# Kernel optimization log

Measured on AMD Instinct MI355X. Metric: run time of the kernel, lower is better.

## Reference

```python
import jax, jax.numpy as jnp
import numpy as np

B, L, DIM, S, K = 2, 2048, 1024, 16, 3
INNER = DIM  # expand = 1 (module only runs with expand=1, see notes)


def setup_inputs() -> dict:
    key = jax.random.key(0)
    ks = jax.random.split(key, 10)
    f = lambda k, shape, s=0.02: jax.random.normal(k, shape, jnp.float32) * s
    return {
        "x": jax.random.normal(ks[0], (B, L, DIM), jnp.float32),
        "gamma": jnp.ones((DIM,), jnp.float32),
        "beta": jnp.zeros((DIM,), jnp.float32),
        "W_in": f(ks[1], (2 * INNER, DIM)),
        "conv_w": f(ks[2], (INNER, 1, K), 0.2),   # depthwise conv, OIL layout
        "W_x": f(ks[3], (2 * S, INNER)),
        "W_dt": f(ks[4], (INNER, DIM)),
        "b_dt": f(ks[5], (INNER,), 0.1),
        "A_log": jax.random.normal(ks[6], (INNER, S), jnp.float32),
        "D_param": jnp.ones((INNER,), jnp.float32),
        "W_out": f(ks[7], (DIM, INNER)),
    }


def reference(x, gamma, beta, W_in, conv_w, W_x, W_dt, b_dt, A_log, D_param, W_out):
    residual = x
    # LayerNorm
    mu = jnp.mean(x, axis=-1, keepdims=True)
    var = jnp.var(x, axis=-1, keepdims=True)
    h = (x - mu) / jnp.sqrt(var + 1e-5) * gamma + beta
    # in_proj + chunk
    xz = jnp.einsum('bld,ed->ble', h, W_in)
    inner = W_in.shape[0] // 2
    xx, z = xz[..., :inner], xz[..., inner:]
    # depthwise conv1d, padding (K-1)//2, no bias
    k = conv_w.shape[-1]
    pad = (k - 1) // 2
    xc = jax.lax.conv_general_dilated(
        xx.transpose(0, 2, 1), conv_w, window_strides=(1,),
        padding=[(pad, pad)], dimension_numbers=('NCL', 'OIL', 'NCL'),
        feature_group_count=inner).transpose(0, 2, 1)
    xc = jax.nn.silu(xc)
    # projections for dt, B, C
    dt = jnp.einsum('bld,ed->ble', xc, W_dt) + b_dt
    BC = jnp.einsum('bld,ed->ble', xc, W_x)
    s = A_log.shape[-1]
    Bm, Cm = BC[..., :s], BC[..., s:]
    # selective scan
    A = -jnp.exp(A_log)                               # (d, s)
    dt = jax.nn.softplus(dt)                          # (b, l, d)
    dA = jnp.exp(jnp.einsum('bld,ds->blds', dt, A))   # (b, l, d, s)
    dB = jnp.einsum('bld,bls->blds', dt, Bm)          # (b, l, d, s)

    def step(state, inputs):
        dA_t, dB_t, C_t = inputs                      # (b,d,s), (b,d,s), (b,s)
        state = state * dA_t + dB_t
        y_t = jnp.einsum('bds,bs->bd', state, C_t)
        return state, y_t

    init = jnp.zeros((x.shape[0], inner, s), xc.dtype)
    _, ys = jax.lax.scan(
        step, init,
        (dA.transpose(1, 0, 2, 3), dB.transpose(1, 0, 2, 3), Cm.transpose(1, 0, 2)))
    y = ys.transpose(1, 0, 2)                         # (b, l, d)
    # skip, gate, out projection, residual
    y = y + D_param * xc
    y = y * jax.nn.silu(z)
    out = jnp.einsum('bld,ed->ble', y, W_out)
    return out + residual
```

## Files before the change

kernel.cpp:

```cpp
#include <hip/hip_runtime.h>
#include <math.h>

#define BB 2
#define LL 2048
#define DIMV 1024
#define SSV 16
#define INNERV 1024
#define E2V 2048
#define MMV (BB*LL)
#define NCHUNK 64
#define CLEN 32

typedef __attribute__((ext_vector_type(8))) short short8;
typedef __attribute__((ext_vector_type(4))) float f32x4;

static __device__ __forceinline__ float4 ld4(const float* p){
  return *reinterpret_cast<const float4*>(p);
}
static __device__ __forceinline__ ushort f2bf(float x){
  unsigned u = __float_as_uint(x);
  unsigned r = (u + 0x7fffu + ((u >> 16) & 1u)) >> 16;
  return (ushort)r;
}
static __device__ __forceinline__ float bf2f(ushort h){
  return __uint_as_float(((unsigned)h) << 16);
}
static __device__ __forceinline__ void gld16(const void* g, void* l){
  __builtin_amdgcn_global_load_lds(
      (const __attribute__((address_space(1))) void*)g,
      (__attribute__((address_space(3))) void*)l, 16, 0, 0);
}

static __device__ __forceinline__ int xcd_swz(){
  int bid = blockIdx.y * gridDim.x + blockIdx.x;
  int nwg = gridDim.x * gridDim.y;
  int q = nwg >> 3, r = nwg & 7;
  int xcd = bid & 7, idx = bid >> 3;
  return (xcd < r ? xcd*(q+1) : r*(q+1) + (xcd - r)*q) + idx;
}

__global__ __launch_bounds__(256) void ln_init(
        const float* __restrict__ x, const float* __restrict__ gamma,
        const float* __restrict__ beta, ushort* __restrict__ hh,
        const float* __restrict__ W_in, const float* __restrict__ W_dt,
        const float* __restrict__ W_out, const float* __restrict__ wx,
        ushort* __restrict__ Wih, ushort* __restrict__ Wch,
        ushort* __restrict__ Woh){
  __shared__ float red[8];
  if (blockIdx.x < 4224){
    int idx = blockIdx.x*256 + threadIdx.x;
    if (idx < 1032*1024){
      const float* src; ushort* dst; int i;
      if (idx < 512*1024){ src = W_in;  dst = Wih; i = idx; }
      else if (idx < 768*1024){ src = W_dt;  dst = Wch; i = idx - 512*1024; }
      else if (idx < 1024*1024){ src = W_out; dst = Woh; i = idx - 768*1024; }
      else { src = wx; dst = Wch + (size_t)1024*1024; i = idx - 1024*1024; }
      float4 v = ld4(src + (size_t)i*4);
      ushort4 H;
      H.x=f2bf(v.x); H.y=f2bf(v.y); H.z=f2bf(v.z); H.w=f2bf(v.w);
      *reinterpret_cast<ushort4*>(dst + (size_t)i*4) = H;
    } else {
      int i = idx - 1032*1024;
      *reinterpret_cast<ushort4*>(Wch + (size_t)1056*1024 + (size_t)i*4) =
          make_ushort4(0,0,0,0);
    }
    return;
  }
  int row = blockIdx.x - 4224;
  int tid = threadIdx.x;
  const float* xr = x + (size_t)row*DIMV;
  float4 v = ld4(xr + tid*4);
  float s  = v.x+v.y+v.z+v.w;
  float s2 = v.x*v.x+v.y*v.y+v.z*v.z+v.w*v.w;
  for (int o=32;o;o>>=1){ s += __shfl_down(s,o); s2 += __shfl_down(s2,o); }
  int wid = tid>>6, lane = tid&63;
  if (lane==0){ red[wid]=s; red[4+wid]=s2; }
  __syncthreads();
  s  = red[0]+red[1]+red[2]+red[3];
  s2 = red[4]+red[5]+red[6]+red[7];
  float mu  = s*(1.f/DIMV);
  float var = s2*(1.f/DIMV) - mu*mu;
  float rstd = rsqrtf(var + 1e-5f);
  float4 g = ld4(gamma + tid*4), be = ld4(beta + tid*4);
  ushort4 H;
  H.x = f2bf((v.x-mu)*rstd*g.x + be.x);
  H.y = f2bf((v.y-mu)*rstd*g.y + be.y);
  H.z = f2bf((v.z-mu)*rstd*g.z + be.z);
  H.w = f2bf((v.w-mu)*rstd*g.w + be.w);
  *reinterpret_cast<ushort4*>(hh + (size_t)row*DIMV + tid*4) = H;
}

#define GBK 64
#define NKT 16

template<int EPI>
static __device__ __forceinline__ void gemm_body(ushort* lds,
    const ushort* __restrict__ A, const ushort* __restrict__ Bw,
    void* __restrict__ Co_, int N, const float* __restrict__ aux,
    float* __restrict__ aux2, int bm, int bn){
  const int t  = threadIdx.x;
  const int rr  = t >> 3;
  const int k16 = (t & 7) ^ (rr & 7);
  const ushort* gA = A  + (size_t)(bm + rr)*1024 + k16*8;
  const ushort* gB = Bw + (size_t)(bn + rr)*1024 + k16*8;
  const int wofs = (t >> 6) * 1024;

  const int l  = t & 63, wv = t >> 6;
  const int wm = wv & 1, wn = wv >> 1;
  const int fr = l & 15, kb = l >> 4;

  f32x4 acc[2][2];
  #pragma unroll
  for (int m=0;m<2;m++){
    #pragma unroll
    for (int n=0;n<2;n++) acc[m][n] = (f32x4){0.f,0.f,0.f,0.f};
  }

  char* Lb0 = (char*)lds;
  char* Lb1 = (char*)lds + 16384;

  #define STAGE_T(base, kt_) { \
    const int ko = (kt_)*GBK; \
    gld16(gA + ko,           (base) +     0 + wofs); \
    gld16(gA + ko + 32*1024, (base) +  4096 + wofs); \
    gld16(gB + ko,           (base) +  8192 + wofs); \
    gld16(gB + ko + 32*1024, (base) + 12288 + wofs); }

  #define COMPUTE_T(base) { \
    short8 a[2][2], b[2][2]; \
    _Pragma("unroll") \
    for (int m=0;m<2;m++){ \
      int row = wm*32 + m*16 + fr; \
      _Pragma("unroll") \
      for (int ks=0;ks<2;ks++) \
        a[m][ks] = *(const short8*)((base) + row*128 + (((ks*4+kb)^(fr&7))*16)); \
    } \
    _Pragma("unroll") \
    for (int n=0;n<2;n++){ \
      int row = wn*32 + n*16 + fr; \
      _Pragma("unroll") \
      for (int ks=0;ks<2;ks++) \
        b[n][ks] = *(const short8*)((base) + 8192 + row*128 + (((ks*4+kb)^(fr&7))*16)); \
    } \
    _Pragma("unroll") \
    for (int ks=0;ks<2;ks++){ \
      _Pragma("unroll") \
      for (int m=0;m<2;m++){ \
        _Pragma("unroll") \
        for (int n=0;n<2;n++) \
          acc[m][n] = __builtin_amdgcn_mfma_f32_16x16x32_bf16(a[m][ks], b[n][ks], acc[m][n], 0,0,0); \
      } \
    } }

  STAGE_T(Lb0, 0);
  __syncthreads();
  #pragma unroll 1
  for (int kt = 0; kt < NKT; kt += 2){
    if (kt+1 < NKT) STAGE_T(Lb1, kt+1);
    COMPUTE_T(Lb0);
    __syncthreads();
    if (kt+1 < NKT){
      if (kt+2 < NKT) STAGE_T(Lb0, kt+2);
      COMPUTE_T(Lb1);
      __syncthreads();
    }
  }
  #undef STAGE_T
  #undef COMPUTE_T

  #pragma unroll
  for (int m=0;m<2;m++){
    int row0 = bm + wm*32 + m*16 + kb*4;
    #pragma unroll
    for (int n=0;n<2;n++){
      int col = bn + wn*32 + n*16 + fr;
      #pragma unroll
      for (int j=0;j<4;j++){
        int r = row0 + j;
        float v = acc[m][n][j];
        if (EPI==0){
          ((ushort*)Co_)[(size_t)r*N + col] = f2bf(v);
        } else if (EPI==2){
          v += aux[(size_t)r*N + col];
          ((float*)Co_)[(size_t)r*N + col] = v;
        } else {
          if (col < 1024){
            v += aux[col];
            v = (v > 20.f) ? v : log1pf(__expf(v));
            ((ushort*)Co_)[(size_t)r*1024 + col] = f2bf(v);
          } else if (col < 1056){
            aux2[(size_t)r*32 + (col - 1024)] = v;
          }
        }
      }
    }
  }
}

template<int EPI>
__global__ __launch_bounds__(256, 4) void gemm_bf16(
    const ushort* __restrict__ A, const ushort* __restrict__ Bw,
    void* __restrict__ Co_, int N, const float* __restrict__ aux){
  __shared__ __align__(16) ushort lds[16384];
  int wg = xcd_swz();
  int row = wg / gridDim.x, col = wg % gridDim.x;
  gemm_body<EPI>(lds, A, Bw, Co_, N, aux, nullptr, row*64, col*64);
}

__global__ __launch_bounds__(256, 4) void gemm_dtbc(
    const ushort* __restrict__ xch, const ushort* __restrict__ Wch,
    ushort* __restrict__ dtb, const float* __restrict__ b_dt,
    float* __restrict__ bcb){
  __shared__ __align__(16) ushort lds[16384];
  int wg = xcd_swz();
  int row = wg / gridDim.x, col = wg % gridDim.x;
  gemm_body<3>(lds, xch, Wch, dtb, 1024, b_dt, bcb, row*64, col*64);
}

__global__ __launch_bounds__(256) void conv_silu_kernel(const ushort* __restrict__ xz,
        const float* __restrict__ cw, ushort* __restrict__ xch){
  int idx = blockIdx.x*256 + threadIdx.x;
  int d4  = idx & 255;
  int row = idx >> 8;
  int t = row & (LL-1);
  const ushort* p = xz + (size_t)row*E2V + d4*4;
  ushort4 u1 = *reinterpret_cast<const ushort4*>(p);
  ushort4 u0 = (t>0)    ? *reinterpret_cast<const ushort4*>(p - E2V) : make_ushort4(0,0,0,0);
  ushort4 u2 = (t<LL-1) ? *reinterpret_cast<const ushort4*>(p + E2V) : make_ushort4(0,0,0,0);
  int d = d4*4;
  float w[12];
  #pragma unroll
  for (int i=0;i<12;i++) w[i] = cw[d*3 + i];
  float4 o;
  o.x = bf2f(u0.x)*w[0] + bf2f(u1.x)*w[1]  + bf2f(u2.x)*w[2];
  o.y = bf2f(u0.y)*w[3] + bf2f(u1.y)*w[4]  + bf2f(u2.y)*w[5];
  o.z = bf2f(u0.z)*w[6] + bf2f(u1.z)*w[7]  + bf2f(u2.z)*w[8];
  o.w = bf2f(u0.w)*w[9] + bf2f(u1.w)*w[10] + bf2f(u2.w)*w[11];
  o.x = o.x / (1.f + __expf(-o.x));
  o.y = o.y / (1.f + __expf(-o.y));
  o.z = o.z / (1.f + __expf(-o.z));
  o.w = o.w / (1.f + __expf(-o.w));
  ushort4 H;
  H.x=f2bf(o.x); H.y=f2bf(o.y); H.z=f2bf(o.z); H.w=f2bf(o.w);
  *reinterpret_cast<ushort4*>(xch + (size_t)row*DIMV + d4*4) = H;
}

__global__ __launch_bounds__(256) void scan_p1(const ushort* __restrict__ dt,
        const float* __restrict__ bc, const float* __restrict__ A_log,
        ushort* __restrict__ F, ushort* __restrict__ P){
  __shared__ float sB[CLEN*32];
  int bid = blockIdx.x;
  int dblk = bid & 3;
  int c  = (bid >> 2) & (NCHUNK-1);
  int b  = bid >> 8;
  int tid = threadIdx.x;
  int d = dblk*256 + tid;
  int row0 = b*LL + c*CLEN;
  ((float4*)sB)[tid] = *((const float4*)(bc + (size_t)row0*32) + tid);
  float a[16];
  {
    const float4* ap = (const float4*)(A_log + d*16);
    #pragma unroll
    for (int q=0;q<4;q++){
      float4 v = ap[q];
      a[q*4+0]=-__expf(v.x); a[q*4+1]=-__expf(v.y);
      a[q*4+2]=-__expf(v.z); a[q*4+3]=-__expf(v.w);
    }
  }
  __syncthreads();
  float st[16];
  #pragma unroll
  for (int s=0;s<16;s++) st[s]=0.f;
  float sdt = 0.f;
  const ushort* dtp = dt + (size_t)row0*DIMV + d;
  for (int t=0;t<CLEN;t++){
    float dtv = bf2f(dtp[(size_t)t*DIMV]);
    sdt += dtv;
    float4 B0 = *(const float4*)&sB[t*32+0];
    float4 B1 = *(const float4*)&sB[t*32+4];
    float4 B2 = *(const float4*)&sB[t*32+8];
    float4 B3 = *(const float4*)&sB[t*32+12];
    float Bv[16] = {B0.x,B0.y,B0.z,B0.w,B1.x,B1.y,B1.z,B1.w,
                    B2.x,B2.y,B2.z,B2.w,B3.x,B3.y,B3.z,B3.w};
    #pragma unroll
    for (int s=0;s<16;s++){
      float dA = __expf(dtv*a[s]);
      st[s] = fmaf(st[s], dA, dtv*Bv[s]);
    }
  }
  size_t o = ((size_t)((b*NCHUNK + c)*DIMV + d))*16;
  #pragma unroll
  for (int q=0;q<4;q++){
    ushort4 fv, pv;
    fv.x=f2bf(st[q*4]);   fv.y=f2bf(st[q*4+1]);
    fv.z=f2bf(st[q*4+2]); fv.w=f2bf(st[q*4+3]);
    pv.x=f2bf(__expf(sdt*a[q*4]));   pv.y=f2bf(__expf(sdt*a[q*4+1]));
    pv.z=f2bf(__expf(sdt*a[q*4+2])); pv.w=f2bf(__expf(sdt*a[q*4+3]));
    *(ushort4*)(F + o + q*4) = fv;
    *(ushort4*)(P + o + q*4) = pv;
  }
}

__global__ __launch_bounds__(256) void scan_p2(const ushort* __restrict__ F,
        const ushort* __restrict__ P, ushort* __restrict__ E){
  int idx = blockIdx.x*256 + threadIdx.x;
  int b  = idx >> 14;
  int ds = idx & 16383;
  float e = 0.f;
  for (int c=0;c<NCHUNK;c++){
    size_t o = ((size_t)(b*NCHUNK + c) << 14) + ds;
    E[o] = f2bf(e);
    e = fmaf(bf2f(P[o]), e, bf2f(F[o]));
  }
}

__global__ __launch_bounds__(256) void scan_p3(const ushort* __restrict__ dt,
        const float* __restrict__ bc, const float* __restrict__ A_log,
        const ushort* __restrict__ E, const ushort* __restrict__ xch,
        const ushort* __restrict__ xz, const float* __restrict__ Dp,
        ushort* __restrict__ yh){
  __shared__ float sBC[CLEN*32];
  int bid = blockIdx.x;
  int dblk = bid & 3;
  int c  = (bid >> 2) & (NCHUNK-1);
  int b  = bid >> 8;
  int tid = threadIdx.x;
  int d = dblk*256 + tid;
  int row0 = b*LL + c*CLEN;
  ((float4*)sBC)[tid] = *((const float4*)(bc + (size_t)row0*32) + tid);
  float a[16];
  {
    const float4* ap = (const float4*)(A_log + d*16);
    #pragma unroll
    for (int q=0;q<4;q++){
      float4 v = ap[q];
      a[q*4+0]=-__expf(v.x); a[q*4+1]=-__expf(v.y);
      a[q*4+2]=-__expf(v.z); a[q*4+3]=-__expf(v.w);
    }
  }
  float st[16];
  {
    size_t o = ((size_t)((b*NCHUNK + c)*DIMV + d))*16;
    #pragma unroll
    for (int q=0;q<4;q++){
      ushort4 v = *(const ushort4*)(E + o + q*4);
      st[q*4]=bf2f(v.x); st[q*4+1]=bf2f(v.y); st[q*4+2]=bf2f(v.z); st[q*4+3]=bf2f(v.w);
    }
  }
  float Dv = Dp[d];
  __syncthreads();
  const ushort* dtp = dt + (size_t)row0*DIMV + d;
  for (int t=0;t<CLEN;t++){
    float dtv = bf2f(dtp[(size_t)t*DIMV]);
    float4 B0 = *(const float4*)&sBC[t*32+0];
    float4 B1 = *(const float4*)&sBC[t*32+4];
    float4 B2 = *(const float4*)&sBC[t*32+8];
    float4 B3 = *(const float4*)&sBC[t*32+12];
    float4 C0 = *(const float4*)&sBC[t*32+16];
    float4 C1 = *(const float4*)&sBC[t*32+20];
    float4 C2 = *(const float4*)&sBC[t*32+24];
    float4 C3 = *(const float4*)&sBC[t*32+28];
    float Bv[16] = {B0.x,B0.y,B0.z,B0.w,B1.x,B1.y,B1.z,B1.w,
                    B2.x,B2.y,B2.z,B2.w,B3.x,B3.y,B3.z,B3.w};
    float Cv[16] = {C0.x,C0.y,C0.z,C0.w,C1.x,C1.y,C1.z,C1.w,
                    C2.x,C2.y,C2.z,C2.w,C3.x,C3.y,C3.z,C3.w};
    float y = 0.f;
    #pragma unroll
    for (int s=0;s<16;s++){
      float dA = __expf(dtv*a[s]);
      st[s] = fmaf(st[s], dA, dtv*Bv[s]);
      y = fmaf(st[s], Cv[s], y);
    }
    int row = row0 + t;
    size_t ofs = (size_t)row*DIMV + d;
    float xcv = bf2f(xch[ofs]);
    float zv  = bf2f(xz[(size_t)row*E2V + INNERV + d]);
    float sz  = zv / (1.f + __expf(-zv));
    yh[ofs] = f2bf((y + Dv*xcv)*sz);
  }
}

extern "C" void kernel_launch(void* const* d_in, const int* in_sizes, int n_in,
                              void* d_out, int out_size, void* d_ws, size_t ws_size,
                              hipStream_t stream){
  const float* x     = (const float*)d_in[0];
  const float* gamma = (const float*)d_in[1];
  const float* beta  = (const float*)d_in[2];
  const float* W_in  = (const float*)d_in[3];
  const float* cw    = (const float*)d_in[4];
  const float* W_x   = (const float*)d_in[5];
  const float* W_dt  = (const float*)d_in[6];
  const float* b_dt  = (const float*)d_in[7];
  const float* A_log = (const float*)d_in[8];
  const float* Dp    = (const float*)d_in[9];
  const float* W_out = (const float*)d_in[10];
  float* out = (float*)d_out;
  float* ws  = (float*)d_ws;
  const size_t MB = (size_t)1 << 20;
  ushort* xzh = (ushort*)ws;
  ushort* hh  = (ushort*)(ws + 4*MB);
  ushort* yh  = (ushort*)(ws + 4*MB);
  ushort* xch = (ushort*)(ws + 6*MB);
  ushort* dtb = (ushort*)(ws + 8*MB);
  ushort* F   = (ushort*)(ws + 10*MB);
  ushort* P   = (ushort*)(ws + 11*MB);
  ushort* E   = (ushort*)(ws + 12*MB);
  ushort* Wih = (ushort*)(ws + 13*MB);
  ushort* Wch = (ushort*)(ws + 14*MB);
  ushort* Woh = (ushort*)(ws + 14*MB + 640*1024);
  float*  bcb = ws + 15*MB + 256*1024;

  ln_init<<<4224 + MMV, 256, 0, stream>>>(x, gamma, beta, hh,
                                          W_in, W_dt, W_out, W_x,
                                          Wih, Wch, Woh);
  gemm_bf16<0><<<dim3(E2V/64, MMV/64), 256, 0, stream>>>(hh, Wih, xzh, E2V, nullptr);
  conv_silu_kernel<<<(MMV*(DIMV/4))/256, 256, 0, stream>>>(xzh, cw, xch);
  gemm_dtbc<<<dim3(18, MMV/64), 256, 0, stream>>>(xch, Wch, dtb, b_dt, bcb);
  scan_p1<<<BB*NCHUNK*(DIMV/256), 256, 0, stream>>>(dtb, bcb, A_log, F, P);
  scan_p2<<<(BB*DIMV*SSV)/256, 256, 0, stream>>>(F, P, E);
  scan_p3<<<BB*NCHUNK*(DIMV/256), 256, 0, stream>>>(dtb, bcb, A_log, E, xch, xzh, Dp, yh);
  gemm_bf16<2><<<dim3(DIMV/64, MMV/64), 256, 0, stream>>>(yh, Woh, out, DIMV, x);
}
```

Before: 147.2 us.

## Keep two GEMM tile loads in flight with explicit vmcnt waits; trim dtbc grid

The bf16 GEMM main loop now issues the first two K-tile stages up front. It then uses s_waitcnt vmcnt(4) and raw s_barrier in place of __syncthreads, so the next stage's global-to-LDS loads overlap compute on the current buffer instead of draining before every barrier. The dt/B/C GEMM grid drops from 18 to 17 column blocks, since 17×64 already covers the 1056 output columns and the extra column of blocks did no useful work. The hand-counted vmcnt depends on each thread issuing exactly four loads per stage; if that count is wrong, the buffers can be read before they are filled.

New measurement: 148.7 us. About the same (+1.1%).

```diff
diff --git a/kernel.cpp b/kernel.cpp
--- a/kernel.cpp
+++ b/kernel.cpp
@@ -31,7 +31,7 @@
       (__attribute__((address_space(3))) void*)l, 16, 0, 0);
 }
 
-static __device__ __forceinline__ int xcd_swz(){
+static __device__ __forceinline__ int xcd_swz2(){
   int bid = blockIdx.y * gridDim.x + blockIdx.x;
   int nwg = gridDim.x * gridDim.y;
   int q = nwg >> 3, r = nwg & 7;
@@ -92,6 +92,10 @@
 
 #define GBK 64
 #define NKT 16
+
+#define WAITV4 asm volatile("s_waitcnt vmcnt(4)" ::: "memory")
+#define WAITV0 asm volatile("s_waitcnt vmcnt(0)" ::: "memory")
+#define WAITL0 asm volatile("s_waitcnt lgkmcnt(0)" ::: "memory")
 
 template<int EPI>
 static __device__ __forceinline__ void gemm_body(ushort* lds,
@@ -153,18 +157,28 @@
     } }
 
   STAGE_T(Lb0, 0);
-  __syncthreads();
+  STAGE_T(Lb1, 1);
   #pragma unroll 1
-  for (int kt = 0; kt < NKT; kt += 2){
-    if (kt+1 < NKT) STAGE_T(Lb1, kt+1);
+  for (int kt = 0; kt < NKT-2; kt += 2){
+    WAITV4;
+    __builtin_amdgcn_s_barrier();
     COMPUTE_T(Lb0);
-    __syncthreads();
-    if (kt+1 < NKT){
-      if (kt+2 < NKT) STAGE_T(Lb0, kt+2);
-      COMPUTE_T(Lb1);
-      __syncthreads();
-    }
-  }
+    WAITL0;
+    __builtin_amdgcn_s_barrier();
+    STAGE_T(Lb0, kt+2);
+    WAITV4;
+    __builtin_amdgcn_s_barrier();
+    COMPUTE_T(Lb1);
+    WAITL0;
+    __builtin_amdgcn_s_barrier();
+    STAGE_T(Lb1, kt+3);
+  }
+  WAITV4;
+  __builtin_amdgcn_s_barrier();
+  COMPUTE_T(Lb0);
+  WAITV0;
+  __builtin_amdgcn_s_barrier();
+  COMPUTE_T(Lb1);
   #undef STAGE_T
   #undef COMPUTE_T
 
@@ -202,7 +216,7 @@
     const ushort* __restrict__ A, const ushort* __restrict__ Bw,
     void* __restrict__ Co_, int N, const float* __restrict__ aux){
   __shared__ __align__(16) ushort lds[16384];
-  int wg = xcd_swz();
+  int wg = xcd_swz2();
   int row = wg / gridDim.x, col = wg % gridDim.x;
   gemm_body<EPI>(lds, A, Bw, Co_, N, aux, nullptr, row*64, col*64);
 }
@@ -212,7 +226,7 @@
     ushort* __restrict__ dtb, const float* __restrict__ b_dt,
     float* __restrict__ bcb){
   __shared__ __align__(16) ushort lds[16384];
-  int wg = xcd_swz();
+  int wg = xcd_swz2();
   int row = wg / gridDim.x, col = wg % gridDim.x;
   gemm_body<3>(lds, xch, Wch, dtb, 1024, b_dt, bcb, row*64, col*64);
 }
@@ -415,7 +429,7 @@
                                           Wih, Wch, Woh);
   gemm_bf16<0><<<dim3(E2V/64, MMV/64), 256, 0, stream>>>(hh, Wih, xzh, E2V, nullptr);
   conv_silu_kernel<<<(MMV*(DIMV/4))/256, 256, 0, stream>>>(xzh, cw, xch);
-  gemm_dtbc<<<dim3(18, MMV/64), 256, 0, stream>>>(xch, Wch, dtb, b_dt, bcb);
+  gemm_dtbc<<<dim3(17, MMV/64), 256, 0, stream>>>(xch, Wch, dtb, b_dt, bcb);
   scan_p1<<<BB*NCHUNK*(DIMV/256), 256, 0, stream>>>(dtb, bcb, A_log, F, P);
   scan_p2<<<(BB*DIMV*SSV)/256, 256, 0, stream>>>(F, P, E);
   scan_p3<<<BB*NCHUNK*(DIMV/256), 256, 0, stream>>>(dtb, bcb, A_log, E, xch, xzh, Dp, yh);
```
